# Performance work log

Hardware: AMD Instinct MI355X
Metric: run time of the kernel (lower is better)

Reference implementation:

```python
import jax, jax.numpy as jnp
import numpy as np

ODIM = 8192      # output dim (slice target)
MSIZE = 64       # tile size
N_BLOCKS = 1024  # size of shared block bank


def setup_inputs() -> dict:
    key = jax.random.key(0)
    k1, k2, k3, k4 = jax.random.split(key, 4)
    x = jax.random.normal(k1, (256, 8192), dtype=jnp.float32)
    # bank of msize x msize module blocks (scaled like fan-in init)
    blocks = jax.random.normal(k2, (N_BLOCKS, MSIZE, MSIZE), dtype=jnp.float32) * 0.02
    bound = 1.0 / np.sqrt(ODIM).astype(np.float32)
    bias = jax.random.uniform(k3, (ODIM,), dtype=jnp.float32, minval=-bound, maxval=bound)
    # parts: [icount, ocount] indices into the block bank
    parts = jax.random.randint(k4, (128, 128), 0, N_BLOCKS)
    return {"x": x, "blocks": blocks, "bias": bias, "parts": parts}


def reference(x, blocks, bias, parts):
    icount, ocount = parts.shape
    m = blocks.shape[-1]
    # build_mosaic: gather blocks per parts and tile into a dense weight matrix
    fc = blocks[parts]                                   # [ic, oc, m, m]
    fc_mat = fc.transpose(0, 2, 1, 3).reshape(icount * m, ocount * m)
    # idim (8192) is divisible by msize, so pad is identity (rem == 0 branch)
    y = x @ fc_mat                                       # [B, oc*m]
    y = y[..., :ODIM] + bias                             # slice + bias; post = Identity
    return y
```

## Files before the change

kernel.cpp:

```cpp
#include <hip/hip_runtime.h>
#include <stdint.h>

#define BATCH 256
#define IDIM  8192
#define ODIM  8192
#define MS    64
#define IC    128
#define OC    128
#define NB    1024

#define TM 128
#define TN 128
#define KSPLIT 4
#define NIB (IC / KSPLIT)

typedef __bf16 bf16x8 __attribute__((ext_vector_type(8)));
typedef float  floatx4 __attribute__((ext_vector_type(4)));

#define WAITCNT_VM(n) ((((n) & 15) | (((n) >> 4) << 14)) | 0x70 | 0xF00)

__device__ __forceinline__ void async_load16(unsigned short* lds_p, const unsigned short* g_p) {
    __builtin_amdgcn_global_load_lds(
        (const __attribute__((address_space(1))) unsigned int*)g_p,
        (__attribute__((address_space(3))) unsigned int*)lds_p,
        16, 0, 0);
}

__device__ __forceinline__ unsigned short f32_to_bf16(float f) {
    unsigned int u = __float_as_uint(f);
    u += 0x7FFFu + ((u >> 16) & 1u);
    return (unsigned short)(u >> 16);
}

#define XCONV_BLKS 1024
#define PT_BLKS 64
__global__ void k_convert(const float* __restrict__ x, const float* __restrict__ blocks,
                          const int* __restrict__ parts,
                          unsigned short* __restrict__ xb, unsigned short* __restrict__ bt,
                          int* __restrict__ pT) {
    __shared__ float tile[MS][MS + 1];
    int b = blockIdx.x;
    if (b < NB) {
        const float4* src4 = (const float4*)(blocks + (size_t)b * MS * MS);
        unsigned short* dst = bt + (size_t)b * MS * MS;
        #pragma unroll
        for (int i = 0; i < 4; ++i) {
            int slot = i * 256 + threadIdx.x;
            int r = slot >> 4, c4 = (slot & 15) * 4;
            float4 v = src4[slot];
            tile[r][c4 + 0] = v.x; tile[r][c4 + 1] = v.y;
            tile[r][c4 + 2] = v.z; tile[r][c4 + 3] = v.w;
        }
        __syncthreads();
        #pragma unroll
        for (int i = 0; i < 2; ++i) {
            int slot = i * 256 + threadIdx.x;
            int c = slot >> 3, o = slot & 7;
            union { unsigned short s[8]; uint4 v; } u;
            #pragma unroll
            for (int j = 0; j < 8; ++j) u.s[j] = f32_to_bf16(tile[o * 8 + j][c]);
            *(uint4*)(dst + c * MS + o * 8) = u.v;
        }
    } else if (b < NB + XCONV_BLKS) {
        int t = (b - NB) * 256 + threadIdx.x;
        const float4* x4 = (const float4*)x;
        float4 a = x4[2 * t], bb = x4[2 * t + 1];
        union { unsigned short s[8]; uint4 v; } u;
        u.s[0] = f32_to_bf16(a.x);  u.s[1] = f32_to_bf16(a.y);
        u.s[2] = f32_to_bf16(a.z);  u.s[3] = f32_to_bf16(a.w);
        u.s[4] = f32_to_bf16(bb.x); u.s[5] = f32_to_bf16(bb.y);
        u.s[6] = f32_to_bf16(bb.z); u.s[7] = f32_to_bf16(bb.w);
        ((uint4*)xb)[t] = u.v;
    } else {
        int t = (b - NB - XCONV_BLKS) * 256 + threadIdx.x;
        int oc = t >> 7, ic = t & 127;
        pT[t] = parts[ic * OC + oc];
    }
}

__global__ __launch_bounds__(256, 2)
void k_mosaic_gemm(const unsigned short* __restrict__ xb,
                   const unsigned short* __restrict__ bt,
                   const int* __restrict__ pT,
                   float* __restrict__ partial) {
    __shared__ __align__(16) unsigned short a_lds[2][TM * MS];
    __shared__ __align__(16) unsigned short b_lds[2][TN * MS];

    const int tid  = threadIdx.x;
    const int lane = tid & 63;
    const int wave = tid >> 6;
    const int wrow = wave >> 1;
    const int wcol = wave & 1;
    const int nt = blockIdx.x;
    const int mt = blockIdx.y;
    const int ks = blockIdx.z;

    const int m0  = mt * TM;
    const int ob0 = nt * 2;
    const int ib0 = ks * NIB;

    const int row  = lane & 15;
    const int quad = lane >> 4;

    int pv0 = 0, pv1 = 0;
    {
        int li = lane & 31;
        pv0 = pT[ob0 * IC + ib0 + li];
        pv1 = pT[(ob0 + 1) * IC + ib0 + li];
    }

    int a_off[2][4], b_off[2][4];
    #pragma unroll
    for (int kk = 0; kk < 2; ++kk) {
        int oct = kk * 4 + quad;
        #pragma unroll
        for (int mi = 0; mi < 4; ++mi) {
            int r = wrow * 64 + mi * 16 + row;
            a_off[kk][mi] = r * MS + ((oct ^ (r & 7)) << 3);
        }
        #pragma unroll
        for (int ni = 0; ni < 4; ++ni) {
            int n = wcol * 64 + ni * 16 + row;
            b_off[kk][ni] = n * MS + ((oct ^ (n & 7)) << 3);
        }
    }

    floatx4 acc[4][4];
    #pragma unroll
    for (int mi = 0; mi < 4; ++mi)
        #pragma unroll
        for (int ni = 0; ni < 4; ++ni)
            acc[mi][ni] = (floatx4){0.f, 0.f, 0.f, 0.f};

#define STAGE(buf, ib_, p0_, p1_) do {                                        \
    _Pragma("unroll")                                                         \
    for (int j = 0; j < 4; ++j) {                                             \
        int slot = j * 256 + tid;                                             \
        int m = slot >> 3;                                                    \
        int oct = (slot & 7) ^ (m & 7);                                       \
        async_load16(&a_lds[buf][slot * 8],                                   \
                     xb + (size_t)(m0 + m) * IDIM + (ib_) * MS + oct * 8);    \
    }                                                                         \
    _Pragma("unroll")                                                         \
    for (int j = 0; j < 4; ++j) {                                             \
        int slot = j * 256 + tid;                                             \
        int n = slot >> 3;                                                    \
        int oct = (slot & 7) ^ (n & 7);                                       \
        int p = (j < 2) ? (p0_) : (p1_);                                      \
        async_load16(&b_lds[buf][slot * 8],                                   \
                     bt + (size_t)p * (MS * MS) + (n & 63) * MS + oct * 8);   \
    } } while (0)

#define COMPUTE(buf) do {                                                     \
    _Pragma("unroll")                                                         \
    for (int kk = 0; kk < 2; ++kk) {                                          \
        bf16x8 af[4], bfr[4];                                                 \
        _Pragma("unroll")                                                     \
        for (int mi = 0; mi < 4; ++mi)                                        \
            af[mi] = *(const bf16x8*)&a_lds[buf][a_off[kk][mi]];              \
        _Pragma("unroll")                                                     \
        for (int ni = 0; ni < 4; ++ni)                                        \
            bfr[ni] = *(const bf16x8*)&b_lds[buf][b_off[kk][ni]];             \
        _Pragma("unroll")                                                     \
        for (int mi = 0; mi < 4; ++mi)                                        \
            _Pragma("unroll")                                                 \
            for (int ni = 0; ni < 4; ++ni)                                    \
                acc[mi][ni] = __builtin_amdgcn_mfma_f32_16x16x32_bf16(        \
                    af[mi], bfr[ni], acc[mi][ni], 0, 0, 0);                   \
    } } while (0)

    {
        int p0 = __shfl(pv0, 0), p1 = __shfl(pv1, 0);
        STAGE(0, ib0 + 0, p0, p1);
    }

    for (int i = 0; i < NIB - 1; ++i) {
        int p0n = __shfl(pv0, i + 1), p1n = __shfl(pv1, i + 1);
        STAGE((i + 1) & 1, ib0 + i + 1, p0n, p1n);
        __builtin_amdgcn_s_waitcnt(WAITCNT_VM(8));
        __builtin_amdgcn_s_barrier();
        COMPUTE(i & 1);
        __builtin_amdgcn_s_barrier();
    }
    __builtin_amdgcn_s_waitcnt(WAITCNT_VM(0));
    __builtin_amdgcn_s_barrier();
    COMPUTE((NIB - 1) & 1);

    float* out = partial + (size_t)ks * BATCH * ODIM;
    #pragma unroll
    for (int mi = 0; mi < 4; ++mi)
        #pragma unroll
        for (int ni = 0; ni < 4; ++ni)
            #pragma unroll
            for (int r = 0; r < 4; ++r) {
                int rowg = m0 + wrow * 64 + mi * 16 + quad * 4 + r;
                int colg = nt * TN + wcol * 64 + ni * 16 + row;
                out[(size_t)rowg * ODIM + colg] = acc[mi][ni][r];
            }
}

__global__ void k_reduce_bias(const float* __restrict__ partial,
                              const float* __restrict__ bias,
                              float* __restrict__ out) {
    int t = blockIdx.x * 256 + threadIdx.x;
    const float4* b4 = (const float4*)bias;
    float4 c = b4[t & (ODIM / 4 - 1)];
    float4 r = {c.x, c.y, c.z, c.w};
    #pragma unroll
    for (int k = 0; k < KSPLIT; ++k) {
        const float4* p = (const float4*)(partial + (size_t)k * BATCH * ODIM);
        float4 a = p[t];
        r.x += a.x; r.y += a.y; r.z += a.z; r.w += a.w;
    }
    ((float4*)out)[t] = r;
}

extern "C" void kernel_launch(void* const* d_in, const int* in_sizes, int n_in,
                              void* d_out, int out_size, void* d_ws, size_t ws_size,
                              hipStream_t stream) {
    const float* x      = (const float*)d_in[0];
    const float* blocks = (const float*)d_in[1];
    const float* bias   = (const float*)d_in[2];
    const int*   parts  = (const int*)d_in[3];
    float* out = (float*)d_out;

    char* ws = (char*)d_ws;
    unsigned short* xb      = (unsigned short*)ws;
    unsigned short* btb     = (unsigned short*)(ws + (4u << 20));
    int*            pTr     = (int*)(ws + (12u << 20));
    float*          partial = (float*)(ws + (13u << 20));

    k_convert<<<NB + XCONV_BLKS + PT_BLKS, 256, 0, stream>>>(x, blocks, parts, xb, btb, pTr);
    k_mosaic_gemm<<<dim3(ODIM / TN, BATCH / TM, KSPLIT), 256, 0, stream>>>(xb, btb, pTr, partial);
    k_reduce_bias<<<(BATCH * ODIM) / (256 * 4), 256, 0, stream>>>(partial, bias, out);
}
```

Before: 120.6 us.

## Use 256x256 output tiles with 1024-thread blocks and 8-way K split

```diff
diff --git a/kernel.cpp b/kernel.cpp
--- a/kernel.cpp
+++ b/kernel.cpp
@@ -9,9 +9,9 @@
 #define OC    128
 #define NB    1024
 
-#define TM 128
-#define TN 128
-#define KSPLIT 4
+#define TM 256
+#define TN 256
+#define KSPLIT 8
 #define NIB (IC / KSPLIT)
 
 typedef __bf16 bf16x8 __attribute__((ext_vector_type(8)));
@@ -78,7 +78,7 @@
     }
 }
 
-__global__ __launch_bounds__(256, 2)
+__global__ __launch_bounds__(1024, 1)
 void k_mosaic_gemm(const unsigned short* __restrict__ xb,
                    const unsigned short* __restrict__ bt,
                    const int* __restrict__ pT,
@@ -89,25 +89,18 @@
     const int tid  = threadIdx.x;
     const int lane = tid & 63;
     const int wave = tid >> 6;
-    const int wrow = wave >> 1;
-    const int wcol = wave & 1;
+    const int wrow = wave >> 2;
+    const int wcol = wave & 3;
     const int nt = blockIdx.x;
-    const int mt = blockIdx.y;
-    const int ks = blockIdx.z;
-
-    const int m0  = mt * TM;
-    const int ob0 = nt * 2;
+    const int ks = blockIdx.y;
+
+    const int ob0 = nt * 4;
     const int ib0 = ks * NIB;
 
     const int row  = lane & 15;
     const int quad = lane >> 4;
 
-    int pv0 = 0, pv1 = 0;
-    {
-        int li = lane & 31;
-        pv0 = pT[ob0 * IC + ib0 + li];
-        pv1 = pT[(ob0 + 1) * IC + ib0 + li];
-    }
+    int pv = pT[(ob0 + (lane >> 4)) * IC + ib0 + (lane & 15)];
 
     int a_off[2][4], b_off[2][4];
     #pragma unroll
@@ -132,21 +125,22 @@
         for (int ni = 0; ni < 4; ++ni)
             acc[mi][ni] = (floatx4){0.f, 0.f, 0.f, 0.f};
 
-#define STAGE(buf, ib_, p0_, p1_) do {                                        \
+#define STAGE(buf, ib_, q0, q1, q2, q3) do {                                  \
     _Pragma("unroll")                                                         \
-    for (int j = 0; j < 4; ++j) {                                             \
-        int slot = j * 256 + tid;                                             \
+    for (int j = 0; j < 2; ++j) {                                             \
+        int slot = j * 1024 + tid;                                            \
         int m = slot >> 3;                                                    \
         int oct = (slot & 7) ^ (m & 7);                                       \
         async_load16(&a_lds[buf][slot * 8],                                   \
-                     xb + (size_t)(m0 + m) * IDIM + (ib_) * MS + oct * 8);    \
+                     xb + (size_t)m * IDIM + (ib_) * MS + oct * 8);           \
     }                                                                         \
     _Pragma("unroll")                                                         \
-    for (int j = 0; j < 4; ++j) {                                             \
-        int slot = j * 256 + tid;                                             \
+    for (int j = 0; j < 2; ++j) {                                             \
+        int slot = j * 1024 + tid;                                            \
         int n = slot >> 3;                                                    \
         int oct = (slot & 7) ^ (n & 7);                                       \
-        int p = (j < 2) ? (p0_) : (p1_);                                      \
+        int p = (j == 0) ? ((tid < 512) ? (q0) : (q1))                        \
+                         : ((tid < 512) ? (q2) : (q3));                       \
         async_load16(&b_lds[buf][slot * 8],                                   \
                      bt + (size_t)p * (MS * MS) + (n & 63) * MS + oct * 8);   \
     } } while (0)
@@ -170,14 +164,15 @@
     } } while (0)
 
     {
-        int p0 = __shfl(pv0, 0), p1 = __shfl(pv1, 0);
-        STAGE(0, ib0 + 0, p0, p1);
+        int q0 = __shfl(pv, 0), q1 = __shfl(pv, 16), q2 = __shfl(pv, 32), q3 = __shfl(pv, 48);
+        STAGE(0, ib0 + 0, q0, q1, q2, q3);
     }
 
     for (int i = 0; i < NIB - 1; ++i) {
-        int p0n = __shfl(pv0, i + 1), p1n = __shfl(pv1, i + 1);
-        STAGE((i + 1) & 1, ib0 + i + 1, p0n, p1n);
-        __builtin_amdgcn_s_waitcnt(WAITCNT_VM(8));
+        int q0 = __shfl(pv, i + 1),      q1 = __shfl(pv, 16 + i + 1);
+        int q2 = __shfl(pv, 32 + i + 1), q3 = __shfl(pv, 48 + i + 1);
+        STAGE((i + 1) & 1, ib0 + i + 1, q0, q1, q2, q3);
+        __builtin_amdgcn_s_waitcnt(WAITCNT_VM(4));
         __builtin_amdgcn_s_barrier();
         COMPUTE(i & 1);
         __builtin_amdgcn_s_barrier();
@@ -193,7 +188,7 @@
         for (int ni = 0; ni < 4; ++ni)
             #pragma unroll
             for (int r = 0; r < 4; ++r) {
-                int rowg = m0 + wrow * 64 + mi * 16 + quad * 4 + r;
+                int rowg = wrow * 64 + mi * 16 + quad * 4 + r;
                 int colg = nt * TN + wcol * 64 + ni * 16 + row;
                 out[(size_t)rowg * ODIM + colg] = acc[mi][ni][r];
             }
@@ -231,6 +226,6 @@
     float*          partial = (float*)(ws + (13u << 20));
 
     k_convert<<<NB + XCONV_BLKS + PT_BLKS, 256, 0, stream>>>(x, blocks, parts, xb, btb, pTr);
-    k_mosaic_gemm<<<dim3(ODIM / TN, BATCH / TM, KSPLIT), 256, 0, stream>>>(xb, btb, pTr, partial);
+    k_mosaic_gemm<<<dim3(ODIM / TN, KSPLIT), 1024, 0, stream>>>(xb, btb, pTr, partial);
     k_reduce_bias<<<(BATCH * ODIM) / (256 * 4), 256, 0, stream>>>(partial, bias, out);
 }
```

Result: slower. 125.5 us (+4.0%).

## Pre-swizzle x into MFMA fragment layout and load A directly to registers

Applied to the files above, without the earlier changes.

```diff
diff --git a/kernel.cpp b/kernel.cpp
--- a/kernel.cpp
+++ b/kernel.cpp
@@ -36,7 +36,7 @@
 #define PT_BLKS 64
 __global__ void k_convert(const float* __restrict__ x, const float* __restrict__ blocks,
                           const int* __restrict__ parts,
-                          unsigned short* __restrict__ xb, unsigned short* __restrict__ bt,
+                          unsigned short* __restrict__ xa, unsigned short* __restrict__ bt,
                           int* __restrict__ pT) {
     __shared__ float tile[MS][MS + 1];
     int b = blockIdx.x;
@@ -62,15 +62,18 @@
             *(uint4*)(dst + c * MS + o * 8) = u.v;
         }
     } else if (b < NB + XCONV_BLKS) {
-        int t = (b - NB) * 256 + threadIdx.x;
-        const float4* x4 = (const float4*)x;
-        float4 a = x4[2 * t], bb = x4[2 * t + 1];
+        int o = (b - NB) * 256 + threadIdx.x;
+        int L = o & 63, kk = (o >> 6) & 1, ib = (o >> 7) & 127, g = o >> 14;
+        int m  = g * 16 + (L & 15);
+        int k0 = ib * 64 + kk * 32 + (L >> 4) * 8;
+        const float* src = x + (size_t)m * IDIM + k0;
+        float4 a = *(const float4*)src, c = *(const float4*)(src + 4);
         union { unsigned short s[8]; uint4 v; } u;
-        u.s[0] = f32_to_bf16(a.x);  u.s[1] = f32_to_bf16(a.y);
-        u.s[2] = f32_to_bf16(a.z);  u.s[3] = f32_to_bf16(a.w);
-        u.s[4] = f32_to_bf16(bb.x); u.s[5] = f32_to_bf16(bb.y);
-        u.s[6] = f32_to_bf16(bb.z); u.s[7] = f32_to_bf16(bb.w);
-        ((uint4*)xb)[t] = u.v;
+        u.s[0] = f32_to_bf16(a.x); u.s[1] = f32_to_bf16(a.y);
+        u.s[2] = f32_to_bf16(a.z); u.s[3] = f32_to_bf16(a.w);
+        u.s[4] = f32_to_bf16(c.x); u.s[5] = f32_to_bf16(c.y);
+        u.s[6] = f32_to_bf16(c.z); u.s[7] = f32_to_bf16(c.w);
+        *(uint4*)(xa + (size_t)o * 8) = u.v;
     } else {
         int t = (b - NB - XCONV_BLKS) * 256 + threadIdx.x;
         int oc = t >> 7, ic = t & 127;
@@ -79,11 +82,10 @@
 }
 
 __global__ __launch_bounds__(256, 2)
-void k_mosaic_gemm(const unsigned short* __restrict__ xb,
+void k_mosaic_gemm(const unsigned short* __restrict__ xa,
                    const unsigned short* __restrict__ bt,
                    const int* __restrict__ pT,
                    float* __restrict__ partial) {
-    __shared__ __align__(16) unsigned short a_lds[2][TM * MS];
     __shared__ __align__(16) unsigned short b_lds[2][TN * MS];
 
     const int tid  = threadIdx.x;
@@ -95,29 +97,21 @@
     const int mt = blockIdx.y;
     const int ks = blockIdx.z;
 
-    const int m0  = mt * TM;
-    const int ob0 = nt * 2;
-    const int ib0 = ks * NIB;
+    const int m0    = mt * TM;
+    const int ob0   = nt * 2;
+    const int ib0   = ks * NIB;
+    const int gbase = mt * 8 + wrow * 4;
 
     const int row  = lane & 15;
     const int quad = lane >> 4;
 
-    int pv0 = 0, pv1 = 0;
-    {
-        int li = lane & 31;
-        pv0 = pT[ob0 * IC + ib0 + li];
-        pv1 = pT[(ob0 + 1) * IC + ib0 + li];
-    }
-
-    int a_off[2][4], b_off[2][4];
+    int pv0 = pT[ob0 * IC + ib0 + (lane & 31)];
+    int pv1 = pT[(ob0 + 1) * IC + ib0 + (lane & 31)];
+
+    int b_off[2][4];
     #pragma unroll
     for (int kk = 0; kk < 2; ++kk) {
         int oct = kk * 4 + quad;
-        #pragma unroll
-        for (int mi = 0; mi < 4; ++mi) {
-            int r = wrow * 64 + mi * 16 + row;
-            a_off[kk][mi] = r * MS + ((oct ^ (r & 7)) << 3);
-        }
         #pragma unroll
         for (int ni = 0; ni < 4; ++ni) {
             int n = wcol * 64 + ni * 16 + row;
@@ -132,15 +126,9 @@
         for (int ni = 0; ni < 4; ++ni)
             acc[mi][ni] = (floatx4){0.f, 0.f, 0.f, 0.f};
 
-#define STAGE(buf, ib_, p0_, p1_) do {                                        \
-    _Pragma("unroll")                                                         \
-    for (int j = 0; j < 4; ++j) {                                             \
-        int slot = j * 256 + tid;                                             \
-        int m = slot >> 3;                                                    \
-        int oct = (slot & 7) ^ (m & 7);                                       \
-        async_load16(&a_lds[buf][slot * 8],                                   \
-                     xb + (size_t)(m0 + m) * IDIM + (ib_) * MS + oct * 8);    \
-    }                                                                         \
+    bf16x8 aA[4][2], aB[4][2];
+
+#define STAGE_B(buf, p0_, p1_) do {                                           \
     _Pragma("unroll")                                                         \
     for (int j = 0; j < 4; ++j) {                                             \
         int slot = j * 256 + tid;                                             \
@@ -151,13 +139,19 @@
                      bt + (size_t)p * (MS * MS) + (n & 63) * MS + oct * 8);   \
     } } while (0)
 
-#define COMPUTE(buf) do {                                                     \
+#define LOAD_A(dst, ib_) do {                                                 \
+    _Pragma("unroll")                                                         \
+    for (int mi = 0; mi < 4; ++mi)                                            \
+    _Pragma("unroll")                                                         \
+    for (int kk = 0; kk < 2; ++kk)                                            \
+        dst[mi][kk] = *(const bf16x8*)(xa +                                   \
+            (((size_t)(gbase + mi) * 128 + (ib_)) * 2 + kk) * 512 + lane * 8);\
+    } while (0)
+
+#define COMPUTE(buf, af) do {                                                 \
     _Pragma("unroll")                                                         \
     for (int kk = 0; kk < 2; ++kk) {                                          \
-        bf16x8 af[4], bfr[4];                                                 \
-        _Pragma("unroll")                                                     \
-        for (int mi = 0; mi < 4; ++mi)                                        \
-            af[mi] = *(const bf16x8*)&a_lds[buf][a_off[kk][mi]];              \
+        bf16x8 bfr[4];                                                        \
         _Pragma("unroll")                                                     \
         for (int ni = 0; ni < 4; ++ni)                                        \
             bfr[ni] = *(const bf16x8*)&b_lds[buf][b_off[kk][ni]];             \
@@ -166,25 +160,35 @@
             _Pragma("unroll")                                                 \
             for (int ni = 0; ni < 4; ++ni)                                    \
                 acc[mi][ni] = __builtin_amdgcn_mfma_f32_16x16x32_bf16(        \
-                    af[mi], bfr[ni], acc[mi][ni], 0, 0, 0);                   \
+                    af[mi][kk], bfr[ni], acc[mi][ni], 0, 0, 0);               \
     } } while (0)
 
+#define ITER(i_, AC, AN) do {                                                 \
+    int it = (i_);                                                            \
+    if (it + 1 < NIB) {                                                       \
+        int q0 = __shfl(pv0, it + 1), q1 = __shfl(pv1, it + 1);               \
+        STAGE_B((it + 1) & 1, q0, q1);                                        \
+        __builtin_amdgcn_sched_barrier(0);                                    \
+        __builtin_amdgcn_s_waitcnt(WAITCNT_VM(4));                            \
+    } else {                                                                  \
+        __builtin_amdgcn_sched_barrier(0);                                    \
+        __builtin_amdgcn_s_waitcnt(WAITCNT_VM(0));                            \
+    }                                                                         \
+    __builtin_amdgcn_s_barrier();                                             \
+    if (it + 1 < NIB) LOAD_A(AN, ib0 + it + 1);                               \
+    COMPUTE(it & 1, AC);                                                      \
+    __builtin_amdgcn_s_barrier();                                             \
+    } while (0)
+
+    LOAD_A(aA, ib0);
     {
-        int p0 = __shfl(pv0, 0), p1 = __shfl(pv1, 0);
-        STAGE(0, ib0 + 0, p0, p1);
-    }
-
-    for (int i = 0; i < NIB - 1; ++i) {
-        int p0n = __shfl(pv0, i + 1), p1n = __shfl(pv1, i + 1);
-        STAGE((i + 1) & 1, ib0 + i + 1, p0n, p1n);
-        __builtin_amdgcn_s_waitcnt(WAITCNT_VM(8));
-        __builtin_amdgcn_s_barrier();
-        COMPUTE(i & 1);
-        __builtin_amdgcn_s_barrier();
-    }
-    __builtin_amdgcn_s_waitcnt(WAITCNT_VM(0));
-    __builtin_amdgcn_s_barrier();
-    COMPUTE((NIB - 1) & 1);
+        int q0 = __shfl(pv0, 0), q1 = __shfl(pv1, 0);
+        STAGE_B(0, q0, q1);
+    }
+    for (int i = 0; i < NIB; i += 2) {
+        ITER(i,     aA, aB);
+        ITER(i + 1, aB, aA);
+    }
 
     float* out = partial + (size_t)ks * BATCH * ODIM;
     #pragma unroll
@@ -225,12 +229,12 @@
     float* out = (float*)d_out;
 
     char* ws = (char*)d_ws;
-    unsigned short* xb      = (unsigned short*)ws;
+    unsigned short* xa      = (unsigned short*)ws;
     unsigned short* btb     = (unsigned short*)(ws + (4u << 20));
     int*            pTr     = (int*)(ws + (12u << 20));
     float*          partial = (float*)(ws + (13u << 20));
 
-    k_convert<<<NB + XCONV_BLKS + PT_BLKS, 256, 0, stream>>>(x, blocks, parts, xb, btb, pTr);
-    k_mosaic_gemm<<<dim3(ODIM / TN, BATCH / TM, KSPLIT), 256, 0, stream>>>(xb, btb, pTr, partial);
+    k_convert<<<NB + XCONV_BLKS + PT_BLKS, 256, 0, stream>>>(x, blocks, parts, xa, btb, pTr);
+    k_mosaic_gemm<<<dim3(ODIM / TN, BATCH / TM, KSPLIT), 256, 0, stream>>>(xa, btb, pTr, partial);
     k_reduce_bias<<<(BATCH * ODIM) / (256 * 4), 256, 0, stream>>>(partial, bias, out);
 }
```

New measurement: 123.3 us. +2.2%, slower.

## Triple-buffer B tiles with asymmetric prefetch depth in mosaic GEMM

Applied to the files above, without the earlier changes.

```diff
diff --git a/kernel.cpp b/kernel.cpp
--- a/kernel.cpp
+++ b/kernel.cpp
@@ -13,6 +13,9 @@
 #define TN 128
 #define KSPLIT 4
 #define NIB (IC / KSPLIT)
+
+#define A_BASE(s) ((s) * 8192)
+#define B_BASE(s) (16384 + (s) * 8192)
 
 typedef __bf16 bf16x8 __attribute__((ext_vector_type(8)));
 typedef float  floatx4 __attribute__((ext_vector_type(4)));
@@ -78,14 +81,13 @@
     }
 }
 
+extern __shared__ unsigned short smem[];
+
 __global__ __launch_bounds__(256, 2)
 void k_mosaic_gemm(const unsigned short* __restrict__ xb,
                    const unsigned short* __restrict__ bt,
                    const int* __restrict__ pT,
                    float* __restrict__ partial) {
-    __shared__ __align__(16) unsigned short a_lds[2][TM * MS];
-    __shared__ __align__(16) unsigned short b_lds[2][TN * MS];
-
     const int tid  = threadIdx.x;
     const int lane = tid & 63;
     const int wave = tid >> 6;
@@ -102,12 +104,8 @@
     const int row  = lane & 15;
     const int quad = lane >> 4;
 
-    int pv0 = 0, pv1 = 0;
-    {
-        int li = lane & 31;
-        pv0 = pT[ob0 * IC + ib0 + li];
-        pv1 = pT[(ob0 + 1) * IC + ib0 + li];
-    }
+    int pv0 = pT[ob0 * IC + ib0 + (lane & 31)];
+    int pv1 = pT[(ob0 + 1) * IC + ib0 + (lane & 31)];
 
     int a_off[2][4], b_off[2][4];
     #pragma unroll
@@ -132,35 +130,37 @@
         for (int ni = 0; ni < 4; ++ni)
             acc[mi][ni] = (floatx4){0.f, 0.f, 0.f, 0.f};
 
-#define STAGE(buf, ib_, p0_, p1_) do {                                        \
+#define STAGE_A(abase, ibx) do {                                              \
     _Pragma("unroll")                                                         \
     for (int j = 0; j < 4; ++j) {                                             \
-        int slot = j * 256 + tid;                                             \
+        int slot = j * 256 + tid;               \
         int m = slot >> 3;                                                    \
         int oct = (slot & 7) ^ (m & 7);                                       \
-        async_load16(&a_lds[buf][slot * 8],                                   \
-                     xb + (size_t)(m0 + m) * IDIM + (ib_) * MS + oct * 8);    \
-    }                                                                         \
+        async_load16(smem + (abase) + slot * 8,                               \
+                     xb + (size_t)(m0 + m) * IDIM + (ibx) * MS + oct * 8);    \
+    } } while (0)
+
+#define STAGE_B(bbase, pa, pb) do {                                           \
     _Pragma("unroll")                                                         \
     for (int j = 0; j < 4; ++j) {                                             \
-        int slot = j * 256 + tid;                                             \
+        int slot = j * 256 + tid;               \
         int n = slot >> 3;                                                    \
         int oct = (slot & 7) ^ (n & 7);                                       \
-        int p = (j < 2) ? (p0_) : (p1_);                                      \
-        async_load16(&b_lds[buf][slot * 8],                                   \
+        int p = (j < 2) ? (pa) : (pb);                                        \
+        async_load16(smem + (bbase) + slot * 8,                               \
                      bt + (size_t)p * (MS * MS) + (n & 63) * MS + oct * 8);   \
     } } while (0)
 
-#define COMPUTE(buf) do {                                                     \
+#define COMPUTE(abase, bbase) do {                                            \
     _Pragma("unroll")                                                         \
     for (int kk = 0; kk < 2; ++kk) {                                          \
         bf16x8 af[4], bfr[4];                                                 \
         _Pragma("unroll")                                                     \
         for (int mi = 0; mi < 4; ++mi)                                        \
-            af[mi] = *(const bf16x8*)&a_lds[buf][a_off[kk][mi]];              \
+            af[mi] = *(const bf16x8*)(smem + (abase) + a_off[kk][mi]);        \
         _Pragma("unroll")                                                     \
         for (int ni = 0; ni < 4; ++ni)                                        \
-            bfr[ni] = *(const bf16x8*)&b_lds[buf][b_off[kk][ni]];             \
+            bfr[ni] = *(const bf16x8*)(smem + (bbase) + b_off[kk][ni]);       \
         _Pragma("unroll")                                                     \
         for (int mi = 0; mi < 4; ++mi)                                        \
             _Pragma("unroll")                                                 \
@@ -169,22 +169,45 @@
                     af[mi], bfr[ni], acc[mi][ni], 0, 0, 0);                   \
     } } while (0)
 
-    {
-        int p0 = __shfl(pv0, 0), p1 = __shfl(pv1, 0);
-        STAGE(0, ib0 + 0, p0, p1);
-    }
-
-    for (int i = 0; i < NIB - 1; ++i) {
-        int p0n = __shfl(pv0, i + 1), p1n = __shfl(pv1, i + 1);
-        STAGE((i + 1) & 1, ib0 + i + 1, p0n, p1n);
-        __builtin_amdgcn_s_waitcnt(WAITCNT_VM(8));
-        __builtin_amdgcn_s_barrier();
-        COMPUTE(i & 1);
-        __builtin_amdgcn_s_barrier();
-    }
+#define ROUND(idx, acS, bcS, asS, bsS) do {                                   \
+    STAGE_A(A_BASE(asS), ib0 + (idx) + 1);                                    \
+    { int q0 = __shfl(pv0, (idx) + 2), q1 = __shfl(pv1, (idx) + 2);           \
+      STAGE_B(B_BASE(bsS), q0, q1); }                                         \
+    __builtin_amdgcn_sched_barrier(0);                                        \
+    __builtin_amdgcn_s_waitcnt(WAITCNT_VM(12));                               \
+    __builtin_amdgcn_s_barrier();                                             \
+    __builtin_amdgcn_sched_barrier(0);                                        \
+    COMPUTE(A_BASE(acS), B_BASE(bcS));                                        \
+    __builtin_amdgcn_sched_barrier(0);                                        \
+    __builtin_amdgcn_s_barrier();                                             \
+    __builtin_amdgcn_sched_barrier(0);                                        \
+    } while (0)
+
+    STAGE_A(A_BASE(0), ib0 + 0);
+    { int q0 = __shfl(pv0, 0), q1 = __shfl(pv1, 0); STAGE_B(B_BASE(0), q0, q1); }
+    { int q0 = __shfl(pv0, 1), q1 = __shfl(pv1, 1); STAGE_B(B_BASE(1), q0, q1); }
+
+    for (int i6 = 0; i6 < 30; i6 += 6) {
+        ROUND(i6 + 0, 0, 0, 1, 2);
+        ROUND(i6 + 1, 1, 1, 0, 0);
+        ROUND(i6 + 2, 0, 2, 1, 1);
+        ROUND(i6 + 3, 1, 0, 0, 2);
+        ROUND(i6 + 4, 0, 1, 1, 0);
+        ROUND(i6 + 5, 1, 2, 0, 1);
+    }
+    STAGE_A(A_BASE(1), ib0 + NIB - 1);
+    __builtin_amdgcn_sched_barrier(0);
+    __builtin_amdgcn_s_waitcnt(WAITCNT_VM(8));
+    __builtin_amdgcn_s_barrier();
+    __builtin_amdgcn_sched_barrier(0);
+    COMPUTE(A_BASE(0), B_BASE(0));
+    __builtin_amdgcn_sched_barrier(0);
+    __builtin_amdgcn_s_barrier();
+    __builtin_amdgcn_sched_barrier(0);
     __builtin_amdgcn_s_waitcnt(WAITCNT_VM(0));
     __builtin_amdgcn_s_barrier();
-    COMPUTE((NIB - 1) & 1);
+    __builtin_amdgcn_sched_barrier(0);
+    COMPUTE(A_BASE(1), B_BASE(1));
 
     float* out = partial + (size_t)ks * BATCH * ODIM;
     #pragma unroll
@@ -230,7 +253,14 @@
     int*            pTr     = (int*)(ws + (12u << 20));
     float*          partial = (float*)(ws + (13u << 20));
 
+    static bool attr_set = false;
+    if (!attr_set) {
+        hipFuncSetAttribute((const void*)k_mosaic_gemm,
+                            hipFuncAttributeMaxDynamicSharedMemorySize, 80 * 1024);
+        attr_set = true;
+    }
+
     k_convert<<<NB + XCONV_BLKS + PT_BLKS, 256, 0, stream>>>(x, blocks, parts, xb, btb, pTr);
-    k_mosaic_gemm<<<dim3(ODIM / TN, BATCH / TM, KSPLIT), 256, 0, stream>>>(xb, btb, pTr, partial);
+    k_mosaic_gemm<<<dim3(ODIM / TN, BATCH / TM, KSPLIT), 256, 80 * 1024, stream>>>(xb, btb, pTr, partial);
     k_reduce_bias<<<(BATCH * ODIM) / (256 * 4), 256, 0, stream>>>(partial, bias, out);
 }
```

Result: no change. 118.8 us (-1.5%).
